# Performance work log

Hardware: AMD Instinct MI355X
Metric: run time of the kernel (lower is better)

Reference implementation:

```python
import jax, jax.numpy as jnp
import numpy as np
import math

B, S, D, H = 2, 2048, 64, 8

def setup_inputs() -> dict:
    key = jax.random.key(0)
    k1, k2, k3, k4 = jax.random.split(key, 4)
    return {
        "x1": jax.random.normal(k1, (B, S, D), dtype=jnp.float32),
        "x2": jax.random.normal(k2, (B, S, D), dtype=jnp.float32),
        "x3": jax.random.normal(k3, (B, H, S, S), dtype=jnp.float32),
        "x4": jax.random.normal(k4, (B, S, D), dtype=jnp.float32),
    }

def reference(x1, x2, x3, x4):
    d = x1.shape[-1]
    # qk: [B,S,S]
    qk = jnp.einsum('bsd,btd->bst', x1, x2) / jnp.sqrt(jnp.asarray(d, x1.dtype))
    # broadcast add bias -> [B,H,S,S]
    scores = qk[:, None, :, :] + x3
    attn = jax.nn.softmax(scores, axis=-1)
    # attn @ x4 with broadcast over H -> [B,H,S,D]
    out = jnp.einsum('bhst,btd->bhsd', attn, x4)
    return out
```

## Files before the change

kernel.cpp:

```cpp
#include <hip/hip_runtime.h>

#define B_ 2
#define S_ 2048
#define D_ 64
#define H_ 8
#define WAVES 4
#define TPW 16

typedef __bf16 bf16x8 __attribute__((ext_vector_type(8)));
typedef float  f32x16 __attribute__((ext_vector_type(16)));
typedef float  f32x4  __attribute__((ext_vector_type(4)));
typedef unsigned int u32x4 __attribute__((ext_vector_type(4)));

#define C_QK 0.18033688011112042f
#define C_B  1.4426950408889634f

__device__ __forceinline__ unsigned int pkbf(float a, float b) {
    __bf16 x = (__bf16)a, y = (__bf16)b;
    unsigned short ux = __builtin_bit_cast(unsigned short, x);
    unsigned short uy = __builtin_bit_cast(unsigned short, y);
    return (unsigned int)ux | ((unsigned int)uy << 16);
}

__global__ __launch_bounds__(256) void attn_kernel(
    const float* __restrict__ x1, const float* __restrict__ x2,
    const float* __restrict__ x3, const float* __restrict__ x4,
    float* __restrict__ out)
{
    __shared__ float sO[WAVES][D_][32];
    __shared__ float sm[WAVES][32];
    __shared__ float sl[WAVES][32];

    const int tid  = threadIdx.x;
    const int w    = tid >> 6;
    const int lane = tid & 63;
    const int lo = lane & 31;
    const int hi = lane >> 5;

    const int bid = blockIdx.x;
    const int b   = bid >> 9;
    const int rem = bid & 511;
    const int h   = rem >> 6;
    const int qt  = rem & 63;
    const int qbase = qt * 32;

    const float* qrow = x1 + ((size_t)b * S_ + qbase + lo) * D_ + 8 * hi;
    bf16x8 Qf[4];
#pragma unroll
    for (int kk = 0; kk < 4; ++kk) {
        f32x4 qa = *(const f32x4*)(qrow + 16 * kk);
        f32x4 qb = *(const f32x4*)(qrow + 16 * kk + 4);
#pragma unroll
        for (int i = 0; i < 4; ++i) {
            Qf[kk][i]     = (__bf16)qa[i];
            Qf[kk][4 + i] = (__bf16)qb[i];
        }
    }

    f32x16 O0, O1;
#pragma unroll
    for (int i = 0; i < 16; ++i) { O0[i] = 0.f; O1[i] = 0.f; }
    float m_run = -3.0e38f;
    float l_run = 0.f;

    const float* brow = x3 + (((size_t)(b * H_ + h) * S_) + qbase + lo) * S_ + 4 * hi;

    auto load_bias = [&](int t, f32x4* dst) {
        const float* p = brow + t * 32;
#pragma unroll
        for (int g = 0; g < 4; ++g) dst[g] = *(const f32x4*)(p + 8 * g);
    };

    auto mk_pfrag = [&](const float* p) -> bf16x8 {
        int a0 = (int)pkbf(p[0], p[1]), a1 = (int)pkbf(p[2], p[3]);
        int b0 = (int)pkbf(p[4], p[5]), b1 = (int)pkbf(p[6], p[7]);
        int s0 = hi ? a0 : b0, s1 = hi ? a1 : b1;
        int r0 = __shfl_xor(s0, 32);
        int r1 = __shfl_xor(s1, 32);
        u32x4 f;
        f[0] = (unsigned int)(hi ? r0 : a0);
        f[1] = (unsigned int)(hi ? r1 : a1);
        f[2] = (unsigned int)(hi ? b0 : r0);
        f[3] = (unsigned int)(hi ? b1 : r1);
        return __builtin_bit_cast(bf16x8, f);
    };

    auto compute = [&](int t, const f32x4* bias) {
        const int tb = t * 32;

        const float* krow = x2 + ((size_t)b * S_ + tb + lo) * D_ + 8 * hi;
        f32x4 kraw[8];
#pragma unroll
        for (int kk = 0; kk < 4; ++kk) {
            kraw[2 * kk]     = *(const f32x4*)(krow + 16 * kk);
            kraw[2 * kk + 1] = *(const f32x4*)(krow + 16 * kk + 4);
        }
        float vraw[4][8];
#pragma unroll
        for (int g2 = 0; g2 < 2; ++g2) {
#pragma unroll
            for (int dh = 0; dh < 2; ++dh) {
                const float* vb = x4 + ((size_t)b * S_ + tb + 16 * g2 + 8 * hi) * D_ + 32 * dh + lo;
#pragma unroll
                for (int i = 0; i < 8; ++i) vraw[2 * g2 + dh][i] = vb[i * D_];
            }
        }

        f32x16 acc;
#pragma unroll
        for (int i = 0; i < 16; ++i) acc[i] = 0.f;
#pragma unroll
        for (int kk = 0; kk < 4; ++kk) {
            bf16x8 kf;
#pragma unroll
            for (int i = 0; i < 4; ++i) {
                kf[i]     = (__bf16)kraw[2 * kk][i];
                kf[4 + i] = (__bf16)kraw[2 * kk + 1][i];
            }
            acc = __builtin_amdgcn_mfma_f32_32x32x16_bf16(kf, Qf[kk], acc, 0, 0, 0);
        }

        float s[16];
#pragma unroll
        for (int r = 0; r < 16; ++r)
            s[r] = acc[r] * C_QK + bias[r >> 2][r & 3] * C_B;

        float pmax = s[0];
#pragma unroll
        for (int r = 1; r < 16; ++r) pmax = fmaxf(pmax, s[r]);
        pmax = fmaxf(pmax, __shfl_xor(pmax, 32));

        if (__any(pmax > m_run)) {
            float mnew = fmaxf(m_run, pmax);
            float sc = __builtin_amdgcn_exp2f(m_run - mnew);
#pragma unroll
            for (int r = 0; r < 16; ++r) { O0[r] *= sc; O1[r] *= sc; }
            l_run *= sc;
            m_run = mnew;
        }

        float p[16];
        float ls = 0.f;
#pragma unroll
        for (int r = 0; r < 16; ++r) {
            p[r] = __builtin_amdgcn_exp2f(s[r] - m_run);
            ls += p[r];
        }
        l_run += ls;

#pragma unroll
        for (int g2 = 0; g2 < 2; ++g2) {
            bf16x8 pf = mk_pfrag(p + 8 * g2);
#pragma unroll
            for (int dh = 0; dh < 2; ++dh) {
                bf16x8 vf;
#pragma unroll
                for (int i = 0; i < 8; ++i) vf[i] = (__bf16)vraw[2 * g2 + dh][i];
                if (dh == 0) O0 = __builtin_amdgcn_mfma_f32_32x32x16_bf16(vf, pf, O0, 0, 0, 0);
                else         O1 = __builtin_amdgcn_mfma_f32_32x32x16_bf16(vf, pf, O1, 0, 0, 0);
            }
        }
    };

    const int t0 = w * TPW;
    f32x4 bA[4], bB[4];
    load_bias(t0, bA);
    for (int t = t0; t < t0 + TPW; t += 2) {
        load_bias(t + 1, bB);
        compute(t, bA);
        if (t + 2 < t0 + TPW) load_bias(t + 2, bA);
        compute(t + 1, bB);
    }

    float l_tot = l_run + __shfl_xor(l_run, 32);
    if (hi == 0) { sm[w][lo] = m_run; sl[w][lo] = l_tot; }
    __syncthreads();

    float M = fmaxf(fmaxf(sm[0][lo], sm[1][lo]), fmaxf(sm[2][lo], sm[3][lo]));
    float scale = __builtin_amdgcn_exp2f(m_run - M);
    float Lsum = 0.f;
#pragma unroll
    for (int w2 = 0; w2 < WAVES; ++w2)
        Lsum += sl[w2][lo] * __builtin_amdgcn_exp2f(sm[w2][lo] - M);

#pragma unroll
    for (int g = 0; g < 4; ++g) {
#pragma unroll
        for (int j = 0; j < 4; ++j) {
            int d = 8 * g + 4 * hi + j;
            sO[w][d][lo]      = O0[4 * g + j] * scale;
            sO[w][d + 32][lo] = O1[4 * g + j] * scale;
        }
    }
    __syncthreads();

    const float inv = 1.0f / Lsum;
    const int d0 = (2 * w + hi) * 8;
    f32x4 r0, r1;
#pragma unroll
    for (int i = 0; i < 4; ++i) {
        float a = sO[0][d0 + i][lo] + sO[1][d0 + i][lo]
                + sO[2][d0 + i][lo] + sO[3][d0 + i][lo];
        float c = sO[0][d0 + 4 + i][lo] + sO[1][d0 + 4 + i][lo]
                + sO[2][d0 + 4 + i][lo] + sO[3][d0 + 4 + i][lo];
        r0[i] = a * inv;
        r1[i] = c * inv;
    }
    float* orow = out + (((size_t)(b * H_ + h) * S_) + qbase + lo) * D_ + d0;
    *(f32x4*)orow       = r0;
    *(f32x4*)(orow + 4) = r1;
}

extern "C" void kernel_launch(void* const* d_in, const int* in_sizes, int n_in,
                              void* d_out, int out_size, void* d_ws, size_t ws_size,
                              hipStream_t stream) {
    const float* x1 = (const float*)d_in[0];
    const float* x2 = (const float*)d_in[1];
    const float* x3 = (const float*)d_in[2];
    const float* x4 = (const float*)d_in[3];
    float* o = (float*)d_out;
    hipLaunchKernelGGL(attn_kernel, dim3(B_ * H_ * (S_ / 32)), dim3(256), 0, stream,
                       x1, x2, x3, x4, o);
}
```

Baseline: 418.1 us.

## Stage bias and K tiles through swizzled LDS for coalesced global loads

```diff
diff --git a/kernel.cpp b/kernel.cpp
--- a/kernel.cpp
+++ b/kernel.cpp
@@ -8,6 +8,7 @@
 #define TPW 16
 
 typedef __bf16 bf16x8 __attribute__((ext_vector_type(8)));
+typedef __bf16 bf16x4 __attribute__((ext_vector_type(4)));
 typedef float  f32x16 __attribute__((ext_vector_type(16)));
 typedef float  f32x4  __attribute__((ext_vector_type(4)));
 typedef unsigned int u32x4 __attribute__((ext_vector_type(4)));
@@ -27,15 +28,17 @@
     const float* __restrict__ x3, const float* __restrict__ x4,
     float* __restrict__ out)
 {
-    __shared__ float sO[WAVES][D_][32];
-    __shared__ float sm[WAVES][32];
-    __shared__ float sl[WAVES][32];
+    __shared__ float smem[8448];
 
     const int tid  = threadIdx.x;
     const int w    = tid >> 6;
     const int lane = tid & 63;
     const int lo = lane & 31;
     const int hi = lane >> 5;
+
+    float*  stg = smem + w * 2048;
+    __bf16* kst = (__bf16*)stg;
+    float*  bst = stg + 1024;
 
     const int bid = blockIdx.x;
     const int b   = bid >> 9;
@@ -63,12 +66,27 @@
     float m_run = -3.0e38f;
     float l_run = 0.f;
 
-    const float* brow = x3 + (((size_t)(b * H_ + h) * S_) + qbase + lo) * S_ + 4 * hi;
-
-    auto load_bias = [&](int t, f32x4* dst) {
-        const float* p = brow + t * 32;
-#pragma unroll
-        for (int g = 0; g < 4; ++g) dst[g] = *(const f32x4*)(p + 8 * g);
+    const int krow_w = lane >> 4;
+    const int kc4    = lane & 15;
+    const int kg8    = kc4 >> 1;
+    const int khalf  = kc4 & 1;
+    const int bq     = lane >> 3;
+    const int bt4    = lane & 7;
+
+    const float* x3base = x3 + ((size_t)(b * H_ + h) * S_ + qbase) * S_;
+
+    auto load_bias_g = [&](int t, f32x4* dst) {
+        const float* base = x3base + t * 32;
+#pragma unroll
+        for (int j = 0; j < 4; ++j)
+            dst[j] = *(const f32x4*)(base + (size_t)(j * 8 + bq) * S_ + 4 * bt4);
+    };
+    auto store_bias = [&](const f32x4* src) {
+#pragma unroll
+        for (int j = 0; j < 4; ++j) {
+            int q = j * 8 + bq;
+            *(f32x4*)(bst + q * 32 + 4 * (bt4 ^ (q & 7))) = src[j];
+        }
     };
 
     auto mk_pfrag = [&](const float* p) -> bf16x8 {
@@ -85,16 +103,13 @@
         return __builtin_bit_cast(bf16x8, f);
     };
 
-    auto compute = [&](int t, const f32x4* bias) {
+    const int t0 = w * TPW;
+    f32x4 bA[4];
+    load_bias_g(t0, bA);
+
+    for (int t = t0; t < t0 + TPW; ++t) {
         const int tb = t * 32;
 
-        const float* krow = x2 + ((size_t)b * S_ + tb + lo) * D_ + 8 * hi;
-        f32x4 kraw[8];
-#pragma unroll
-        for (int kk = 0; kk < 4; ++kk) {
-            kraw[2 * kk]     = *(const f32x4*)(krow + 16 * kk);
-            kraw[2 * kk + 1] = *(const f32x4*)(krow + 16 * kk + 4);
-        }
         float vraw[4][8];
 #pragma unroll
         for (int g2 = 0; g2 < 2; ++g2) {
@@ -106,24 +121,45 @@
             }
         }
 
+        const float* kbase = x2 + ((size_t)b * S_ + tb) * D_;
+        f32x4 kreg[8];
+#pragma unroll
+        for (int j = 0; j < 8; ++j)
+            kreg[j] = *(const f32x4*)(kbase + j * 256 + lane * 4);
+
+        store_bias(bA);
+        {
+            int tn = (t + 1 < t0 + TPW) ? t + 1 : t0;
+            load_bias_g(tn, bA);
+        }
+
+#pragma unroll
+        for (int j = 0; j < 8; ++j) {
+            bf16x4 kb;
+            kb[0] = (__bf16)kreg[j][0]; kb[1] = (__bf16)kreg[j][1];
+            kb[2] = (__bf16)kreg[j][2]; kb[3] = (__bf16)kreg[j][3];
+            int row = j * 4 + krow_w;
+            *(bf16x4*)(kst + row * 64 + 8 * (kg8 ^ (row & 7)) + 4 * khalf) = kb;
+        }
+
         f32x16 acc;
 #pragma unroll
         for (int i = 0; i < 16; ++i) acc[i] = 0.f;
 #pragma unroll
         for (int kk = 0; kk < 4; ++kk) {
-            bf16x8 kf;
-#pragma unroll
-            for (int i = 0; i < 4; ++i) {
-                kf[i]     = (__bf16)kraw[2 * kk][i];
-                kf[4 + i] = (__bf16)kraw[2 * kk + 1][i];
-            }
+            bf16x8 kf = *(const bf16x8*)(kst + lo * 64 + 8 * ((2 * kk + hi) ^ (lo & 7)));
             acc = __builtin_amdgcn_mfma_f32_32x32x16_bf16(kf, Qf[kk], acc, 0, 0, 0);
         }
 
+        f32x4 rB[4];
+#pragma unroll
+        for (int g = 0; g < 4; ++g)
+            rB[g] = *(const f32x4*)(bst + lo * 32 + 4 * ((2 * g + hi) ^ (lo & 7)));
+
         float s[16];
 #pragma unroll
         for (int r = 0; r < 16; ++r)
-            s[r] = acc[r] * C_QK + bias[r >> 2][r & 3] * C_B;
+            s[r] = acc[r] * C_QK + rB[r >> 2][r & 3] * C_B;
 
         float pmax = s[0];
 #pragma unroll
@@ -160,36 +196,28 @@
                 else         O1 = __builtin_amdgcn_mfma_f32_32x32x16_bf16(vf, pf, O1, 0, 0, 0);
             }
         }
-    };
-
-    const int t0 = w * TPW;
-    f32x4 bA[4], bB[4];
-    load_bias(t0, bA);
-    for (int t = t0; t < t0 + TPW; t += 2) {
-        load_bias(t + 1, bB);
-        compute(t, bA);
-        if (t + 2 < t0 + TPW) load_bias(t + 2, bA);
-        compute(t + 1, bB);
     }
 
     float l_tot = l_run + __shfl_xor(l_run, 32);
-    if (hi == 0) { sm[w][lo] = m_run; sl[w][lo] = l_tot; }
+    if (hi == 0) { smem[8192 + w * 32 + lo] = m_run; smem[8320 + w * 32 + lo] = l_tot; }
     __syncthreads();
 
-    float M = fmaxf(fmaxf(sm[0][lo], sm[1][lo]), fmaxf(sm[2][lo], sm[3][lo]));
+    float M = fmaxf(fmaxf(smem[8192 + lo], smem[8192 + 32 + lo]),
+                    fmaxf(smem[8192 + 64 + lo], smem[8192 + 96 + lo]));
     float scale = __builtin_amdgcn_exp2f(m_run - M);
     float Lsum = 0.f;
 #pragma unroll
     for (int w2 = 0; w2 < WAVES; ++w2)
-        Lsum += sl[w2][lo] * __builtin_amdgcn_exp2f(sm[w2][lo] - M);
-
+        Lsum += smem[8320 + w2 * 32 + lo] * __builtin_amdgcn_exp2f(smem[8192 + w2 * 32 + lo] - M);
+
+    float* sO = smem;
 #pragma unroll
     for (int g = 0; g < 4; ++g) {
 #pragma unroll
         for (int j = 0; j < 4; ++j) {
             int d = 8 * g + 4 * hi + j;
-            sO[w][d][lo]      = O0[4 * g + j] * scale;
-            sO[w][d + 32][lo] = O1[4 * g + j] * scale;
+            sO[(w * D_ + d) * 32 + lo]        = O0[4 * g + j] * scale;
+            sO[(w * D_ + d + 32) * 32 + lo]   = O1[4 * g + j] * scale;
         }
     }
     __syncthreads();
@@ -199,10 +227,10 @@
     f32x4 r0, r1;
 #pragma unroll
     for (int i = 0; i < 4; ++i) {
-        float a = sO[0][d0 + i][lo] + sO[1][d0 + i][lo]
-                + sO[2][d0 + i][lo] + sO[3][d0 + i][lo];
-        float c = sO[0][d0 + 4 + i][lo] + sO[1][d0 + 4 + i][lo]
-                + sO[2][d0 + 4 + i][lo] + sO[3][d0 + 4 + i][lo];
+        float a = sO[(0 * D_ + d0 + i) * 32 + lo] + sO[(1 * D_ + d0 + i) * 32 + lo]
+                + sO[(2 * D_ + d0 + i) * 32 + lo] + sO[(3 * D_ + d0 + i) * 32 + lo];
+        float c = sO[(0 * D_ + d0 + 4 + i) * 32 + lo] + sO[(1 * D_ + d0 + 4 + i) * 32 + lo]
+                + sO[(2 * D_ + d0 + 4 + i) * 32 + lo] + sO[(3 * D_ + d0 + 4 + i) * 32 + lo];
         r0[i] = a * inv;
         r1[i] = c * inv;
     }
```

Measured after the change: 387.9 us. 1.08x faster.
